# Performance work log

Measured on AMD Instinct MI355X. Metric: run time of the kernel, lower is better.

The kernel has to match this reference:

```python
import jax, jax.numpy as jnp
import numpy as np
from jax import lax

B, C, H, W = 16, 128, 64, 64
S = 16  # d_state


def setup_inputs() -> dict:
    key = jax.random.key(0)
    ks = jax.random.split(key, 12)
    d = {
        'x': jax.random.normal(ks[0], (B, C, H, W), jnp.float32),
        'conv_w': jax.random.normal(ks[1], (C, C, 3, 3), jnp.float32) * (1.0 / np.sqrt(C * 9)),
        'conv_b': jax.random.normal(ks[2], (C,), jnp.float32) * 0.01,
        'dt_w': jax.random.normal(ks[3], (C, C), jnp.float32) * (1.0 / np.sqrt(C)),
        'dt_b': jax.random.normal(ks[4], (C,), jnp.float32) * 0.01,
        'A': jax.random.normal(ks[5], (C, S), jnp.float32),
        'D': jax.random.normal(ks[6], (C,), jnp.float32),
        'g1_w': jax.random.normal(ks[7], (C, C), jnp.float32) * (1.0 / np.sqrt(C)),
        'g1_b': jax.random.normal(ks[8], (C,), jnp.float32) * 0.01,
        'g2_w': jax.random.normal(ks[9], (C, C), jnp.float32) * (1.0 / np.sqrt(C)),
        'g2_b': jax.random.normal(ks[10], (C,), jnp.float32) * 0.01,
    }
    return d


def _forward(x, conv_w, conv_b, dt_w, dt_b, A, D, g1_w, g1_b, g2_w, g2_b):
    identity = x
    # 3x3 conv, padding=1 (SAME)
    x = lax.conv_general_dilated(x, conv_w, (1, 1), 'SAME',
                                 dimension_numbers=('NCHW', 'OIHW', 'NCHW'))
    x = x + conv_b[None, :, None, None]
    # spectral gate: global avg pool -> 1x1 conv -> relu -> 1x1 conv -> sigmoid
    pooled = jnp.mean(x, axis=(2, 3))                       # [B, C]
    g = jax.nn.relu(jnp.einsum('bc,oc->bo', pooled, g1_w) + g1_b)
    g = jax.nn.sigmoid(jnp.einsum('bc,oc->bo', g, g2_w) + g2_b)
    x = x * g[:, :, None, None]
    # ssm scan over H*W tokens
    x_seq = x.transpose(0, 2, 3, 1).reshape(x.shape[0], H * W, C)  # [B, L, C]
    dt = jax.nn.sigmoid(jnp.einsum('blc,oc->blo', x_seq, dt_w) + dt_b)
    An = -jnp.exp(A)   # [C, S]
    Dp = jnp.exp(D)    # [C]

    def step(h, inp):
        xt, dtt = inp  # each [B, C]
        h = h * jnp.exp(An[None] * dtt[:, :, None]) + xt[:, :, None]  # [B, C, S]
        y = jnp.sum(h * An[None], axis=-1) + Dp * xt                   # [B, C]
        return h, y

    h0 = jnp.zeros((x.shape[0], C, S), x.dtype)
    xs = (x_seq.transpose(1, 0, 2), dt.transpose(1, 0, 2))  # [L, B, C]
    _, ys = lax.scan(step, h0, xs)                           # ys: [L, B, C]
    y = ys.transpose(1, 0, 2).reshape(x.shape[0], H, W, C).transpose(0, 3, 1, 2)
    return y + identity


def reference(x, conv_w, conv_b, dt_w, dt_b, A, D, g1_w, g1_b, g2_w, g2_b):
    return _forward(x, conv_w, conv_b, dt_w, dt_b, A, D, g1_w, g1_b, g2_w, g2_b)
```

## Files before the change

### kernel.cpp

```cpp
#include <hip/hip_runtime.h>
#include <hip/hip_bf16.h>
#include <stdint.h>

#define BB 16
#define CC 128
#define HH 64
#define WW 64
#define LL 4096
#define SS 16
#define NCH 64
#define CT 64

typedef __attribute__((ext_vector_type(4))) float f32x4;
typedef __attribute__((ext_vector_type(8))) short short8;
typedef __attribute__((ext_vector_type(4))) unsigned int u32x4;

#define AS1 __attribute__((address_space(1)))
#define AS3 __attribute__((address_space(3)))

__device__ __forceinline__ float bf2f(unsigned short u) {
    union { unsigned int i; float f; } v;
    v.i = ((unsigned int)u) << 16;
    return v.f;
}
__device__ __forceinline__ unsigned short f2bf(float f) {
    union { float f; unsigned int i; } v;
    v.f = f;
    unsigned int x = v.i;
    return (unsigned short)((x + 0x7fffu + ((x >> 16) & 1u)) >> 16);
}
__device__ __forceinline__ float fexp2(float x) { return __builtin_amdgcn_exp2f(x); }

__global__ void k0a(const float* __restrict__ conv_w, const float* __restrict__ dt_w,
                    const float* __restrict__ A, const float* __restrict__ Dv,
                    short* __restrict__ wf, short* __restrict__ wdtf,
                    float* __restrict__ An, float* __restrict__ An2, float* __restrict__ Dp) {
    int idx = blockIdx.x * 256 + threadIdx.x;
    if (idx < 18432) {
        int lane = idx & 63, fr = idx >> 6;
        int nfg = fr & 7, ks = (fr >> 3) & 3, tp = fr >> 5;
        int dy = tp / 3, dx = tp % 3;
        int cout = nfg * 16 + (lane & 15);
        int cin0 = ks * 32 + (lane >> 4) * 8;
        short8 v;
#pragma unroll
        for (int j = 0; j < 8; ++j)
            v[j] = (short)f2bf(conv_w[((cout * CC + cin0 + j) * 3 + dy) * 3 + dx]);
        *(short8*)(wf + (size_t)idx * 8) = v;
    } else if (idx < 20480) {
        int i2 = idx - 18432;
        int lane = i2 & 63, fr = i2 >> 6;
        int nfg = fr & 7, ks = fr >> 3;
        int o = nfg * 16 + (lane & 15);
        int c0 = ks * 32 + (lane >> 4) * 8;
        short8 v;
#pragma unroll
        for (int j = 0; j < 8; ++j) v[j] = (short)f2bf(dt_w[o * CC + c0 + j]);
        *(short8*)(wdtf + (size_t)i2 * 8) = v;
    } else if (idx < 22528) {
        int i3 = idx - 20480;
        float a = -expf(A[i3]);
        An[i3] = a;
        An2[i3] = a * 1.4426950408889634f;
    } else if (idx < 22656) {
        int c = idx - 22528;
        Dp[c] = expf(Dv[c]);
    }
}

__global__ __launch_bounds__(256) void k0b(const float* __restrict__ x, unsigned short* __restrict__ xT) {
    __shared__ float lt[64][65];
    int bid = blockIdx.x;
    int b = bid >> 7, rem = bid & 127;
    int tt = rem >> 1, ct = rem & 1;
    int t0 = tt * 64, c0 = ct * 64;
    int tid = threadIdx.x;
    int colr = tid & 63, rowb = tid >> 6;
#pragma unroll
    for (int r = 0; r < 16; ++r) {
        int row = rowb + r * 4;
        lt[row][colr] = x[(size_t)(b * CC + c0 + row) * LL + t0 + colr];
    }
    __syncthreads();
#pragma unroll
    for (int r = 0; r < 16; ++r) {
        int trow = rowb + r * 4;
        xT[((size_t)b * LL + t0 + trow) * CC + c0 + colr] = f2bf(lt[colr][trow]);
    }
}

__global__ __launch_bounds__(256) void k1(const unsigned short* __restrict__ xT,
                                          const short* __restrict__ wf,
                                          const float* __restrict__ conv_b,
                                          unsigned short* __restrict__ convT,
                                          float* __restrict__ pooled) {
    __shared__ __align__(16) unsigned short slab[3 * 66 * 128];
    int bid = blockIdx.x;
    int b = bid >> 6, h = bid & 63;
    int tid = threadIdx.x;
    int wave = tid >> 6, lane = tid & 63;

    if (tid < 96) {
        int dy = tid >> 5, r = (tid >> 4) & 1, j = tid & 15;
        u32x4 z = {0, 0, 0, 0};
        *(u32x4*)((char*)slab + dy * 16896 + (r ? 16640 : 0) + j * 16) = z;
    }
#pragma unroll
    for (int dy = 0; dy < 3; ++dy) {
        int hs = h + dy - 1;
        char* slabdy = (char*)slab + dy * 16896;
        if (hs >= 0 && hs < HH) {
            const char* src = (const char*)xT + (size_t)(b * LL + hs * 64) * 256;
#pragma unroll
            for (int i = 0; i < 4; ++i) {
                unsigned int Xbase = 256u + (unsigned)i * 4096u + (unsigned)wave * 1024u;
                unsigned int X = Xbase + (unsigned)lane * 16u;
                unsigned int tok = X >> 8;
                unsigned int srcoff = ((X & ~255u) - 256u) | ((X & 255u) ^ ((tok & 7u) << 4));
                __builtin_amdgcn_global_load_lds((const AS1 unsigned int*)(src + srcoff),
                                                 (AS3 unsigned int*)(slabdy + Xbase), 16, 0, 0);
            }
        } else {
            u32x4 z = {0, 0, 0, 0};
#pragma unroll
            for (int i = 0; i < 4; ++i)
                *(u32x4*)(slabdy + 256 + tid * 64 + i * 16) = z;
        }
    }
    __syncthreads();

    int lm = lane & 15, lg = lane >> 4;
    f32x4 acc[4][2];
#pragma unroll
    for (int m = 0; m < 4; ++m)
#pragma unroll
        for (int n = 0; n < 2; ++n) acc[m][n] = (f32x4){0.f, 0.f, 0.f, 0.f};

#pragma unroll
    for (int tp = 0; tp < 9; ++tp) {
        int dy = tp / 3, dx = tp % 3;
        const char* slabdy = (const char*)slab + dy * 16896;
#pragma unroll
        for (int ks = 0; ks < 4; ++ks) {
            short8 bf0 = *(const short8*)(wf + ((size_t)(((tp * 4 + ks) * 8) + wave * 2 + 0) * 64 + lane) * 8);
            short8 bf1 = *(const short8*)(wf + ((size_t)(((tp * 4 + ks) * 8) + wave * 2 + 1) * 64 + lane) * 8);
#pragma unroll
            for (int mf = 0; mf < 4; ++mf) {
                int tok = mf * 16 + lm + dx;
                unsigned int off = (unsigned)((tok * 256 + ks * 64 + lg * 16) ^ ((tok & 7) << 4));
                short8 af = *(const short8*)(slabdy + off);
                acc[mf][0] = __builtin_amdgcn_mfma_f32_16x16x32_bf16(af, bf0, acc[mf][0], 0, 0, 0);
                acc[mf][1] = __builtin_amdgcn_mfma_f32_16x16x32_bf16(af, bf1, acc[mf][1], 0, 0, 0);
            }
        }
    }

    int n0w = wave * 32;
    size_t tokbase = (size_t)(b * LL + h * 64);
    float psum[2] = {0.f, 0.f};
#pragma unroll
    for (int nf = 0; nf < 2; ++nf) {
        int n = n0w + nf * 16 + lm;
        float bias = conv_b[n];
#pragma unroll
        for (int mf = 0; mf < 4; ++mf)
#pragma unroll
            for (int r = 0; r < 4; ++r) {
                int w = mf * 16 + lg * 4 + r;
                float v = acc[mf][nf][r] + bias;
                convT[(tokbase + w) * CC + n] = f2bf(v);
                psum[nf] += v;
            }
    }
#pragma unroll
    for (int nf = 0; nf < 2; ++nf) {
        float s = psum[nf];
        s += __shfl_xor(s, 16);
        s += __shfl_xor(s, 32);
        if (lane < 16) atomicAdd(&pooled[b * CC + n0w + nf * 16 + lane], s);
    }
}

__global__ __launch_bounds__(128) void k2(const float* __restrict__ pooled, const float* __restrict__ g1w,
                                          const float* __restrict__ g1b, const float* __restrict__ g2w,
                                          const float* __restrict__ g2b, float* __restrict__ gate) {
    __shared__ float wl[128 * 129];
    __shared__ float meanr[128];
    __shared__ float garr[128];
    int b = blockIdx.x;
    int tid = threadIdx.x;
    meanr[tid] = pooled[b * CC + tid] * (1.f / 4096.f);
#pragma unroll 4
    for (int i = 0; i < 128; ++i) wl[i * 129 + tid] = g1w[i * 128 + tid];
    __syncthreads();
    float acc = g1b[tid];
    for (int c = 0; c < 128; ++c) acc += meanr[c] * wl[tid * 129 + c];
    garr[tid] = fmaxf(acc, 0.f);
    __syncthreads();
#pragma unroll 4
    for (int i = 0; i < 128; ++i) wl[i * 129 + tid] = g2w[i * 128 + tid];
    __syncthreads();
    float acc2 = g2b[tid];
    for (int c = 0; c < 128; ++c) acc2 += garr[c] * wl[tid * 129 + c];
    gate[b * CC + tid] = __builtin_amdgcn_rcpf(1.f + fexp2(-1.4426950408889634f * acc2));
}

__global__ __launch_bounds__(256) void k3(const unsigned short* __restrict__ convT,
                                          const short* __restrict__ wdtf,
                                          const float* __restrict__ gate,
                                          const float* __restrict__ dt_b,
                                          unsigned short* __restrict__ dtT) {
    __shared__ __align__(16) unsigned short albuf[128 * 128];
    __shared__ float gl[128];
    int bid = blockIdx.x;
    int b = bid >> 5, t0 = (bid & 31) * 128;
    int tid = threadIdx.x;
    int wave = tid >> 6, lane = tid & 63;
    if (tid < 128) gl[tid] = gate[b * CC + tid];
    __syncthreads();
    const char* srcb = (const char*)convT + (size_t)(b * LL + t0) * 256;
#pragma unroll
    for (int i = 0; i < 8; ++i) {
        unsigned int byteoff = (unsigned)((i * 256 + tid) * 16);
        unsigned int tok = byteoff >> 8;
        unsigned int inner = byteoff & 255u;
        int c8 = (int)(inner >> 1);
        short8 v = *(const short8*)(srcb + (size_t)tok * 256 + inner);
#pragma unroll
        for (int j = 0; j < 8; ++j) {
            float f = bf2f((unsigned short)v[j]) * gl[c8 + j];
            v[j] = (short)f2bf(f);
        }
        *(short8*)((char*)albuf + (byteoff ^ ((tok & 7u) << 4))) = v;
    }
    __syncthreads();

    int lm = lane & 15, lg = lane >> 4;
    f32x4 acc[8][2];
#pragma unroll
    for (int m = 0; m < 8; ++m)
#pragma unroll
        for (int n = 0; n < 2; ++n) acc[m][n] = (f32x4){0.f, 0.f, 0.f, 0.f};
#pragma unroll
    for (int ks = 0; ks < 4; ++ks) {
        short8 bf0 = *(const short8*)(wdtf + ((size_t)((ks * 8) + wave * 2 + 0) * 64 + lane) * 8);
        short8 bf1 = *(const short8*)(wdtf + ((size_t)((ks * 8) + wave * 2 + 1) * 64 + lane) * 8);
#pragma unroll
        for (int mf = 0; mf < 8; ++mf) {
            int tok = mf * 16 + lm;
            unsigned int off = (unsigned)((tok * 256 + ks * 64 + lg * 16) ^ ((tok & 7) << 4));
            short8 af = *(const short8*)((const char*)albuf + off);
            acc[mf][0] = __builtin_amdgcn_mfma_f32_16x16x32_bf16(af, bf0, acc[mf][0], 0, 0, 0);
            acc[mf][1] = __builtin_amdgcn_mfma_f32_16x16x32_bf16(af, bf1, acc[mf][1], 0, 0, 0);
        }
    }
#pragma unroll
    for (int nf = 0; nf < 2; ++nf) {
        int o = wave * 32 + nf * 16 + lm;
        float zb = dt_b[o];
#pragma unroll
        for (int mf = 0; mf < 8; ++mf)
#pragma unroll
            for (int r = 0; r < 4; ++r) {
                int tok = mf * 16 + lg * 4 + r;
                float z = acc[mf][nf][r] + zb;
                float d = __builtin_amdgcn_rcpf(1.f + fexp2(-1.4426950408889634f * z));
                dtT[(size_t)(b * LL + t0 + tok) * CC + o] = f2bf(d);
            }
    }
}

__global__ __launch_bounds__(128) void k4(const unsigned short* __restrict__ convT,
                                          const unsigned short* __restrict__ dtT,
                                          const float* __restrict__ gate,
                                          const float* __restrict__ An2,
                                          float* __restrict__ hend, float* __restrict__ decay) {
    int bid = blockIdx.x;
    int b = bid >> 6, ch = bid & 63;
    int c = threadIdx.x;
    float a2[SS], h[SS];
#pragma unroll
    for (int s = 0; s < SS; ++s) {
        a2[s] = An2[c * SS + s];
        h[s] = 0.f;
    }
    float g = gate[b * CC + c];
    float sdt = 0.f;
    int t0 = ch * CT;
    const unsigned short* xp = convT + (size_t)(b * LL + t0) * CC + c;
    const unsigned short* dp = dtT + (size_t)(b * LL + t0) * CC + c;
#pragma unroll 4
    for (int t = 0; t < CT; ++t) {
        float x = bf2f(xp[t * CC]) * g;
        float d = bf2f(dp[t * CC]);
        sdt += d;
#pragma unroll
        for (int s = 0; s < SS; ++s) h[s] = h[s] * fexp2(a2[s] * d) + x;
    }
    size_t base = ((size_t)(b * NCH + ch) * CC + c) * SS;
#pragma unroll
    for (int s = 0; s < SS; ++s) {
        hend[base + s] = h[s];
        decay[base + s] = fexp2(a2[s] * sdt);
    }
}

__global__ __launch_bounds__(256) void k5(const float* __restrict__ hend, const float* __restrict__ decay,
                                          float* __restrict__ H0) {
    int idx = blockIdx.x * 256 + threadIdx.x;
    int b = idx >> 11, rem = idx & 2047;
    float Hv = 0.f;
    for (int k = 0; k < NCH; ++k) {
        size_t base = (size_t)(b * NCH + k) * 2048 + rem;
        H0[base] = Hv;
        Hv = hend[base] + Hv * decay[base];
    }
}

__global__ __launch_bounds__(128) void k6(const unsigned short* __restrict__ convT,
                                          const unsigned short* __restrict__ dtT,
                                          const float* __restrict__ gate,
                                          const float* __restrict__ Antab,
                                          const float* __restrict__ An2tab,
                                          const float* __restrict__ Dp,
                                          const float* __restrict__ H0,
                                          const float* __restrict__ xin,
                                          float* __restrict__ out) {
    __shared__ float ylds[128][65];
    int bid = blockIdx.x;
    int b = bid >> 6, ch = bid & 63;
    int c = threadIdx.x;
    float a2[SS], an[SS], h[SS];
#pragma unroll
    for (int s = 0; s < SS; ++s) {
        a2[s] = An2tab[c * SS + s];
        an[s] = Antab[c * SS + s];
    }
    size_t hbase = ((size_t)(b * NCH + ch) * CC + c) * SS;
#pragma unroll
    for (int s = 0; s < SS; ++s) h[s] = H0[hbase + s];
    float g = gate[b * CC + c];
    float dpc = Dp[c];
    int t0 = ch * CT;
    const unsigned short* xp = convT + (size_t)(b * LL + t0) * CC + c;
    const unsigned short* dp = dtT + (size_t)(b * LL + t0) * CC + c;
#pragma unroll 4
    for (int t = 0; t < CT; ++t) {
        float x = bf2f(xp[t * CC]) * g;
        float d = bf2f(dp[t * CC]);
        float y = dpc * x;
#pragma unroll
        for (int s = 0; s < SS; ++s) {
            h[s] = h[s] * fexp2(a2[s] * d) + x;
            y += h[s] * an[s];
        }
        ylds[c][t] = y;
    }
    __syncthreads();
    int tt = c & 63, rh = c >> 6;
    size_t outbase = (size_t)b * CC * LL + t0 + tt;
#pragma unroll 4
    for (int rr = 0; rr < 64; ++rr) {
        int row = rr * 2 + rh;
        size_t gi = outbase + (size_t)row * LL;
        out[gi] = ylds[row][tt] + xin[gi];
    }
}

extern "C" void kernel_launch(void* const* d_in, const int* in_sizes, int n_in,
                              void* d_out, int out_size, void* d_ws, size_t ws_size,
                              hipStream_t stream) {
    const float* x      = (const float*)d_in[0];
    const float* conv_w = (const float*)d_in[1];
    const float* conv_b = (const float*)d_in[2];
    const float* dt_w   = (const float*)d_in[3];
    const float* dt_b   = (const float*)d_in[4];
    const float* A      = (const float*)d_in[5];
    const float* D      = (const float*)d_in[6];
    const float* g1w    = (const float*)d_in[7];
    const float* g1b    = (const float*)d_in[8];
    const float* g2w    = (const float*)d_in[9];
    const float* g2b    = (const float*)d_in[10];

    char* ws = (char*)d_ws;
    unsigned short* xT    = (unsigned short*)(ws + 0);
    float* hend           = (float*)(ws + 0);
    float* decay          = (float*)(ws + 8388608);
    unsigned short* convT = (unsigned short*)(ws + 16777216);
    unsigned short* dtT   = (unsigned short*)(ws + 33554432);
    float* H0             = (float*)(ws + 50331648);
    short* wf             = (short*)(ws + 58720256);
    short* wdtf           = (short*)(ws + 59015168);
    float* pooled         = (float*)(ws + 59047936);
    float* gate           = (float*)(ws + 59056128);
    float* Antab          = (float*)(ws + 59064320);
    float* An2tab         = (float*)(ws + 59072512);
    float* Dp             = (float*)(ws + 59080704);
    float* outp           = (float*)d_out;

    hipMemsetAsync(pooled, 0, BB * CC * sizeof(float), stream);
    hipLaunchKernelGGL(k0a, dim3(89), dim3(256), 0, stream, conv_w, dt_w, A, D, wf, wdtf, Antab, An2tab, Dp);
    hipLaunchKernelGGL(k0b, dim3(2048), dim3(256), 0, stream, x, xT);
    hipLaunchKernelGGL(k1, dim3(1024), dim3(256), 0, stream, xT, wf, conv_b, convT, pooled);
    hipLaunchKernelGGL(k2, dim3(16), dim3(128), 0, stream, pooled, g1w, g1b, g2w, g2b, gate);
    hipLaunchKernelGGL(k3, dim3(512), dim3(256), 0, stream, convT, wdtf, gate, dt_b, dtT);
    hipLaunchKernelGGL(k4, dim3(1024), dim3(128), 0, stream, convT, dtT, gate, An2tab, hend, decay);
    hipLaunchKernelGGL(k5, dim3(128), dim3(256), 0, stream, hend, decay, H0);
    hipLaunchKernelGGL(k6, dim3(1024), dim3(128), 0, stream, convT, dtT, gate, Antab, An2tab, Dp, H0, x, outp);
}
```

Baseline: 143.5 us.

## Fuse chunk-scan pass into dt projection kernel and fold pooled memset into setup

The per-chunk SSM scan (k4) now runs inside k3 and reads the gated conv activations and dt values from shared memory instead of reloading them from global memory. Each 256-thread block covers two 64-token chunks, one per thread half. The pooled buffer zeroing moves from a memset into the setup kernel, which removes one launch, and the chunk-end state writes are vectorised. The costs are extra LDS per block (about 34KB more), which may lower occupancy, and the scan using only 128 blocks' worth of parallel chunks per batch at the same width as before.

```diff
diff --git a/kernel.cpp b/kernel.cpp
--- a/kernel.cpp
+++ b/kernel.cpp
@@ -34,7 +34,8 @@
 __global__ void k0a(const float* __restrict__ conv_w, const float* __restrict__ dt_w,
                     const float* __restrict__ A, const float* __restrict__ Dv,
                     short* __restrict__ wf, short* __restrict__ wdtf,
-                    float* __restrict__ An, float* __restrict__ An2, float* __restrict__ Dp) {
+                    float* __restrict__ An, float* __restrict__ An2, float* __restrict__ Dp,
+                    float* __restrict__ pooled) {
     int idx = blockIdx.x * 256 + threadIdx.x;
     if (idx < 18432) {
         int lane = idx & 63, fr = idx >> 6;
@@ -65,6 +66,8 @@
     } else if (idx < 22656) {
         int c = idx - 22528;
         Dp[c] = expf(Dv[c]);
+    } else if (idx < 24704) {
+        pooled[idx - 22656] = 0.f;
     }
 }
 
@@ -209,11 +212,14 @@
                                           const short* __restrict__ wdtf,
                                           const float* __restrict__ gate,
                                           const float* __restrict__ dt_b,
-                                          unsigned short* __restrict__ dtT) {
+                                          const float* __restrict__ An2,
+                                          unsigned short* __restrict__ dtT,
+                                          float* __restrict__ hend, float* __restrict__ decay) {
     __shared__ __align__(16) unsigned short albuf[128 * 128];
+    __shared__ __align__(16) unsigned short dtl[128 * 136];
     __shared__ float gl[128];
     int bid = blockIdx.x;
-    int b = bid >> 5, t0 = (bid & 31) * 128;
+    int b = bid >> 5, tile = bid & 31, t0 = tile * 128;
     int tid = threadIdx.x;
     int wave = tid >> 6, lane = tid & 63;
     if (tid < 128) gl[tid] = gate[b * CC + tid];
@@ -265,43 +271,43 @@
                 int tok = mf * 16 + lg * 4 + r;
                 float z = acc[mf][nf][r] + zb;
                 float d = __builtin_amdgcn_rcpf(1.f + fexp2(-1.4426950408889634f * z));
-                dtT[(size_t)(b * LL + t0 + tok) * CC + o] = f2bf(d);
+                unsigned short ub = f2bf(d);
+                dtT[(size_t)(b * LL + t0 + tok) * CC + o] = ub;
+                dtl[tok * 136 + o] = ub;
             }
     }
-}
-
-__global__ __launch_bounds__(128) void k4(const unsigned short* __restrict__ convT,
-                                          const unsigned short* __restrict__ dtT,
-                                          const float* __restrict__ gate,
-                                          const float* __restrict__ An2,
-                                          float* __restrict__ hend, float* __restrict__ decay) {
-    int bid = blockIdx.x;
-    int b = bid >> 6, ch = bid & 63;
-    int c = threadIdx.x;
+    __syncthreads();
+
+    int half = tid >> 7, c = tid & 127;
+    int ch = tile * 2 + half;
     float a2[SS], h[SS];
 #pragma unroll
     for (int s = 0; s < SS; ++s) {
         a2[s] = An2[c * SS + s];
         h[s] = 0.f;
     }
-    float g = gate[b * CC + c];
     float sdt = 0.f;
-    int t0 = ch * CT;
-    const unsigned short* xp = convT + (size_t)(b * LL + t0) * CC + c;
-    const unsigned short* dp = dtT + (size_t)(b * LL + t0) * CC + c;
 #pragma unroll 4
     for (int t = 0; t < CT; ++t) {
-        float x = bf2f(xp[t * CC]) * g;
-        float d = bf2f(dp[t * CC]);
+        int tokb = half * 64 + t;
+        unsigned int xoff = ((unsigned)(tokb * 256 + c * 2)) ^ (((unsigned)tokb & 7u) << 4);
+        float x = bf2f(*(const unsigned short*)((const char*)albuf + xoff));
+        float d = bf2f(dtl[tokb * 136 + c]);
         sdt += d;
 #pragma unroll
         for (int s = 0; s < SS; ++s) h[s] = h[s] * fexp2(a2[s] * d) + x;
     }
     size_t base = ((size_t)(b * NCH + ch) * CC + c) * SS;
 #pragma unroll
-    for (int s = 0; s < SS; ++s) {
-        hend[base + s] = h[s];
-        decay[base + s] = fexp2(a2[s] * sdt);
+    for (int q = 0; q < 4; ++q) {
+        f32x4 hv, dv;
+#pragma unroll
+        for (int j = 0; j < 4; ++j) {
+            hv[j] = h[q * 4 + j];
+            dv[j] = fexp2(a2[q * 4 + j] * sdt);
+        }
+        *(f32x4*)(hend + base + q * 4) = hv;
+        *(f32x4*)(decay + base + q * 4) = dv;
     }
 }
 
@@ -398,13 +404,11 @@
     float* Dp             = (float*)(ws + 59080704);
     float* outp           = (float*)d_out;
 
-    hipMemsetAsync(pooled, 0, BB * CC * sizeof(float), stream);
-    hipLaunchKernelGGL(k0a, dim3(89), dim3(256), 0, stream, conv_w, dt_w, A, D, wf, wdtf, Antab, An2tab, Dp);
+    hipLaunchKernelGGL(k0a, dim3(97), dim3(256), 0, stream, conv_w, dt_w, A, D, wf, wdtf, Antab, An2tab, Dp, pooled);
     hipLaunchKernelGGL(k0b, dim3(2048), dim3(256), 0, stream, x, xT);
     hipLaunchKernelGGL(k1, dim3(1024), dim3(256), 0, stream, xT, wf, conv_b, convT, pooled);
     hipLaunchKernelGGL(k2, dim3(16), dim3(128), 0, stream, pooled, g1w, g1b, g2w, g2b, gate);
-    hipLaunchKernelGGL(k3, dim3(512), dim3(256), 0, stream, convT, wdtf, gate, dt_b, dtT);
-    hipLaunchKernelGGL(k4, dim3(1024), dim3(128), 0, stream, convT, dtT, gate, An2tab, hend, decay);
+    hipLaunchKernelGGL(k3, dim3(512), dim3(256), 0, stream, convT, wdtf, gate, dt_b, An2tab, dtT, hend, decay);
     hipLaunchKernelGGL(k5, dim3(128), dim3(256), 0, stream, hend, decay, H0);
     hipLaunchKernelGGL(k6, dim3(1024), dim3(128), 0, stream, convT, dtT, gate, Antab, An2tab, Dp, H0, x, outp);
 }
```

New measurement: 135.1 us. -5.8%, faster.
